# Performance work log

Hardware: AMD Instinct MI355X
Metric: run time of the kernel (lower is better)

## Reference

```python
import jax, jax.numpy as jnp
from jax import lax
import numpy as np

HF, WF, CIN, CONV_C, A, STRIDE = 100, 160, 512, 512, 9, 16
NEG = -1e9
IOU_THR = 0.7


def _make_anchor_map(hf, wf, stride):
    # (cy, cx, h, w) per anchor, 9 anchors: scales {64,128,256} x ratios {0.5,1,2}
    cy = (np.arange(hf, dtype=np.float32) + 0.5) * stride
    cx = (np.arange(wf, dtype=np.float32) + 0.5) * stride
    sizes = np.array([[s * np.sqrt(r), s / np.sqrt(r)]
                      for s in (64.0, 128.0, 256.0) for r in (0.5, 1.0, 2.0)],
                     dtype=np.float32)  # [9,2] = (h,w)
    cyg, cxg = np.meshgrid(cy, cx, indexing='ij')  # [hf,wf]
    am = np.zeros((hf, wf, A, 4), np.float32)
    am[..., 0] = cyg[..., None]
    am[..., 1] = cxg[..., None]
    am[..., 2] = sizes[:, 0]
    am[..., 3] = sizes[:, 1]
    return jnp.asarray(am.reshape(1, hf, wf, 4 * A))


def _conv(x, w, b, pad):
    y = lax.conv_general_dilated(x, w, (1, 1), pad,
                                 dimension_numbers=('NHWC', 'HWIO', 'NHWC'))
    return y + b


def _nms(boxes, scores, max_out, iou_thr):
    # jit-friendly fixed-size NMS; index computation is non-differentiable.
    bx = lax.stop_gradient(boxes)
    y1, x1, y2, x2 = bx[:, 0], bx[:, 1], bx[:, 2], bx[:, 3]
    areas = (y2 - y1) * (x2 - x1)

    def step(sc, _):
        best = jnp.argmax(sc)
        ok = sc[best] > NEG * 0.5
        b = bx[best]
        iy1 = jnp.maximum(y1, b[0]); ix1 = jnp.maximum(x1, b[1])
        iy2 = jnp.minimum(y2, b[2]); ix2 = jnp.minimum(x2, b[3])
        inter = jnp.maximum(iy2 - iy1, 0.0) * jnp.maximum(ix2 - ix1, 0.0)
        iou = inter / (areas + areas[best] - inter + 1e-8)
        sc = jnp.where((iou > iou_thr) & ok, NEG, sc)
        sc = sc.at[best].set(NEG)
        return sc, (best, ok)

    _, (keep, valid) = lax.scan(step, lax.stop_gradient(scores), None, length=max_out)
    return jnp.where(valid[:, None], boxes[keep], 0.0)  # [max_out,4], zero-padded


def setup_inputs() -> dict:
    key = jax.random.key(0)
    ks = jax.random.split(key, 6)
    image = jax.random.normal(ks[0], (1, HF * STRIDE, WF * STRIDE, 3), jnp.float32)
    feature_map = jax.random.normal(ks[1], (1, HF, WF, CIN), jnp.float32)
    anchor_map = _make_anchor_map(HF, WF, STRIDE)
    W1 = jax.random.normal(ks[2], (3, 3, CIN, CONV_C), jnp.float32) * 0.01
    b1 = jnp.zeros((CONV_C,), jnp.float32)
    Wc = jax.random.normal(ks[3], (1, 1, CONV_C, A), jnp.float32) * 0.01
    bc = jnp.zeros((A,), jnp.float32)
    Wr = jax.random.normal(ks[4], (1, 1, CONV_C, 4 * A), jnp.float32) * 0.01
    br = jnp.zeros((4 * A,), jnp.float32)
    return {'image': image, 'feature_map': feature_map, 'anchor_map': anchor_map,
            'W1': W1, 'b1': b1, 'Wc': Wc, 'bc': bc, 'Wr': Wr, 'br': br, 'training': 0}


def reference(image, feature_map, anchor_map, W1, b1, Wc, bc, Wr, br, training):
    pre_nms, post_nms = ((12000, 2000) if training else (6000, 300))
    # conv heads
    y = jax.nn.relu(_conv(feature_map, W1, b1, 'SAME'))
    scores_map = jax.nn.softmax(_conv(y, Wc, bc, 'SAME'), axis=-1)   # [1,HF,WF,9]
    delta_map = _conv(y, Wr, br, 'SAME')                              # [1,HF,WF,36]
    # flatten (_extract)
    anchors = anchor_map.reshape(-1, 4)        # (cy,cx,h,w)
    scores = scores_map.reshape(-1)            # [N]
    box_deltas = delta_map.reshape(-1, 4)      # (ty,tx,th,tw)
    # deltas_to_bboxes (means=0, stds=1)
    ctr = anchors[:, :2] + box_deltas[:, :2] * anchors[:, 2:]
    sz = anchors[:, 2:] * jnp.exp(box_deltas[:, 2:])
    proposals = jnp.concatenate([ctr - 0.5 * sz, ctr + 0.5 * sz], axis=1)  # (y1,x1,y2,x2)
    # sort desc + pre-NMS top-k
    top_scores, top_idx = lax.top_k(scores, pre_nms)
    proposals = proposals[top_idx]
    # clip to image
    h = jnp.float32(image.shape[1]); w = jnp.float32(image.shape[2])
    tl = jnp.maximum(proposals[:, 0:2], 0.0)
    y2 = jnp.minimum(proposals[:, 2], h)[:, None]
    x2 = jnp.minimum(proposals[:, 3], w)[:, None]
    proposals = jnp.concatenate([tl, y2, x2], axis=1)
    # size filter (mask instead of gather; NMS skips masked boxes)
    height = proposals[:, 2] - proposals[:, 0]
    width = proposals[:, 3] - proposals[:, 1]
    valid = (height >= 16.0) & (width >= 16.0)
    nms_scores = jnp.where(valid, top_scores, NEG)
    out_props = _nms(proposals, nms_scores, post_nms, IOU_THR)
    return (scores_map, box_deltas, out_props)
```

## Files before the change

### kernel.cpp

```cpp
#include <hip/hip_runtime.h>
#include <math.h>

#define HF 100
#define WFD 160
#define CIN 512
#define CONV_C 512
#define NPIX (HF*WFD)
#define NBOX (NPIX*9)
#define PRE_NMS 6000
#define POST_NMS 300
#define NEGV (-1.0e9f)
#define IMG_H 1600.0f
#define IMG_W 2560.0f
#define NHBINS 32768
#define NWORDS 94
#define NSORT 6016

#define PR 102
#define PC 162
#define NPAD ((size_t)PR*PC*512)

typedef __attribute__((ext_vector_type(8))) _Float16 half8;
typedef __attribute__((ext_vector_type(4))) float floatx4;

__device__ __forceinline__ unsigned short f2h_hi(float x) {
    _Float16 h = (_Float16)x;
    return __builtin_bit_cast(unsigned short, h);
}
__device__ __forceinline__ unsigned short f2h_lo(float x, unsigned short hbits) {
    _Float16 h = __builtin_bit_cast(_Float16, hbits);
    _Float16 l = (_Float16)((x - (float)h) * 2048.0f);
    return __builtin_bit_cast(unsigned short, l);
}

#define GLL16(g, l) __builtin_amdgcn_global_load_lds( \
    (const __attribute__((address_space(1))) void*)(g), \
    (__attribute__((address_space(3))) void*)(l), 16, 0, 0)

static const size_t OYREG = 0;
static const size_t OXH   = OYREG + (size_t)NPIX * CONV_C;
static const size_t OXL   = OXH + NPAD / 2;
static const size_t OWH   = OXL + NPAD / 2;
static const size_t OWL   = OWH + (size_t)9*512*512/2;
static const size_t ORAW  = OWL + (size_t)9*512*512/2;
static const size_t ONMS  = ORAW + NBOX;
static const size_t OPY1  = ONMS + NBOX;
static const size_t OPX1  = OPY1 + NBOX;
static const size_t OPY2  = OPX1 + NBOX;
static const size_t OPX2  = OPY2 + NBOX;
static const size_t OHIST = OPX2 + NBOX;
static const size_t OCNT  = OHIST + NHBINS;
static const size_t OPAR  = OCNT + 4;
static const size_t OCS   = OPAR + 2;
static const size_t OCY1  = OCS + PRE_NMS;
static const size_t OCX1  = OCY1 + PRE_NMS;
static const size_t OCY2  = OCX1 + PRE_NMS;
static const size_t OCX2  = OCY2 + PRE_NMS;
static const size_t OW2H  = OCX2 + PRE_NMS;
static const size_t OW2L  = OW2H + 12288;
static const size_t OMASK = OXH;
static const size_t OSY1  = OXL;
static const size_t OSX1  = OSY1 + NSORT;
static const size_t OSY2  = OSX1 + NSORT;
static const size_t OSX2  = OSY2 + NSORT;
static const size_t OSAR  = OSX2 + NSORT;

__global__ __launch_bounds__(256) void split_x(
    const float* __restrict__ X,
    unsigned short* __restrict__ Xh, unsigned short* __restrict__ Xl)
{
    const int idx = blockIdx.x * 256 + threadIdx.x;
    const int p = idx >> 7;
    const int kq = (idx & 127) * 4;
    const float4 v = *(const float4*)(X + (size_t)p * 512 + kq);
    const int r = p / WFD, c = p % WFD;
    const size_t dst = ((size_t)(r + 1) * PC + (c + 1)) * 512 + kq;
    float vv[4] = { v.x, v.y, v.z, v.w };
    unsigned short h[4], lo[4];
    #pragma unroll
    for (int u = 0; u < 4; ++u) {
        h[u]  = f2h_hi(vv[u]);
        lo[u] = f2h_lo(vv[u], h[u]);
    }
    uint2 ph, pl;
    ph.x = (unsigned)h[0]  | ((unsigned)h[1]  << 16);
    ph.y = (unsigned)h[2]  | ((unsigned)h[3]  << 16);
    pl.x = (unsigned)lo[0] | ((unsigned)lo[1] << 16);
    pl.y = (unsigned)lo[2] | ((unsigned)lo[3] << 16);
    *(uint2*)(Xh + dst) = ph;
    *(uint2*)(Xl + dst) = pl;
}

__global__ __launch_bounds__(256) void split_w(
    const float* __restrict__ W1,
    unsigned short* __restrict__ Wh, unsigned short* __restrict__ Wl)
{
    __shared__ unsigned short Lh[64 * 64];
    __shared__ unsigned short Ll[64 * 64];
    const int t = threadIdx.x;
    const int dydx = blockIdx.x >> 6;
    const int rem  = blockIdx.x & 63;
    const int k0 = (rem >> 3) * 64, n0 = (rem & 7) * 64;

    #pragma unroll
    for (int i = 0; i < 4; ++i) {
        const int f = t + 256 * i;
        const int row = f >> 4;
        const int cp  = (f & 15) * 4;
        const float4 v = *(const float4*)(W1 + ((size_t)(dydx * 512 + k0 + row)) * 512 + n0 + cp);
        float vv[4] = { v.x, v.y, v.z, v.w };
        #pragma unroll
        for (int u = 0; u < 4; ++u) {
            const unsigned short h = f2h_hi(vv[u]);
            Lh[(cp + u) * 64 + row] = h;
            Ll[(cp + u) * 64 + row] = f2h_lo(vv[u], h);
        }
    }
    __syncthreads();
    const int n  = t >> 2;
    const int kp = (t & 3) * 16;
    const size_t gbase = ((size_t)(dydx * 512 + n0 + n)) * 512 + k0 + kp;
    *(uint4*)(Wh + gbase)     = *(const uint4*)(Lh + n * 64 + kp);
    *(uint4*)(Wh + gbase + 8) = *(const uint4*)(Lh + n * 64 + kp + 8);
    *(uint4*)(Wl + gbase)     = *(const uint4*)(Ll + n * 64 + kp);
    *(uint4*)(Wl + gbase + 8) = *(const uint4*)(Ll + n * 64 + kp + 8);
}

__global__ __launch_bounds__(256) void split_w2(
    const float* __restrict__ Wc, const float* __restrict__ Wr,
    unsigned short* __restrict__ W2h, unsigned short* __restrict__ W2l)
{
    const int i = blockIdx.x * 256 + threadIdx.x;
    if (i >= 48 * 512) return;
    const int n = i >> 9, k = i & 511;
    float v = 0.f;
    if (n < 9) v = Wc[k * 9 + n];
    else if (n < 45) v = Wr[k * 36 + (n - 9)];
    const unsigned short h = f2h_hi(v);
    W2h[i] = h;
    W2l[i] = f2h_lo(v, h);
}

__global__ __launch_bounds__(256, 2) void conv_mfma(
    const unsigned short* __restrict__ Xh, const unsigned short* __restrict__ Xl,
    const unsigned short* __restrict__ Wh, const unsigned short* __restrict__ Wl,
    const float* __restrict__ b1,
    unsigned short* __restrict__ Yh, unsigned short* __restrict__ Yl)
{
    __shared__ alignas(16) unsigned short Ah[2][128 * 32];
    __shared__ alignas(16) unsigned short Al[2][128 * 32];
    __shared__ alignas(16) unsigned short Bh[2][128 * 32];
    __shared__ alignas(16) unsigned short Bl[2][128 * 32];

    const int tid = threadIdx.x;
    const int w = tid >> 6, l = tid & 63;
    const int wy = w >> 1, wx = w & 1;

    const int bx = blockIdx.x;
    const int q = bx & 7, s5 = bx >> 3;
    const int tile = (q < 5) ? (q * 16 + s5) : (80 + (q - 5) * 15 + s5);
    const int pm0 = tile * 128, oc0 = blockIdx.y * 128;

    const int swW = ((l & 3) ^ ((l >> 3) & 3)) * 8;
    int aoff[2], boff[2], ldsOff[2];
    #pragma unroll
    for (int i = 0; i < 2; ++i) {
        const int m = w * 32 + i * 16 + (l >> 2);
        const int p = pm0 + m;
        const int r = p / WFD, c = p % WFD;
        aoff[i] = ((r + 1) * PC + (c + 1)) * 512 + swW;
        boff[i] = (oc0 + m) * 512 + swW;
        ldsOff[i] = (w * 32 + i * 16) * 32;
    }

    const int swR = (((l >> 4) ^ ((l >> 1) & 3))) * 8;
    int afrag[4], bfrag[4];
    #pragma unroll
    for (int i = 0; i < 4; ++i) {
        afrag[i] = (wy * 64 + i * 16 + (l & 15)) * 32 + swR;
        bfrag[i] = (wx * 64 + i * 16 + (l & 15)) * 32 + swR;
    }

    floatx4 acc[4][4], accL[4][4];
    #pragma unroll
    for (int j = 0; j < 4; ++j) {
        const float bv = b1[oc0 + wx * 64 + j * 16 + (l & 15)];
        #pragma unroll
        for (int i = 0; i < 4; ++i) {
            acc[i][j][0] = bv; acc[i][j][1] = bv; acc[i][j][2] = bv; acc[i][j][3] = bv;
            accL[i][j][0] = 0.f; accL[i][j][1] = 0.f; accL[i][j][2] = 0.f; accL[i][j][3] = 0.f;
        }
    }

    #define CSTAGE(bf, dAx, dBx)                                    \
        _Pragma("unroll")                                           \
        for (int i = 0; i < 2; ++i) {                               \
            GLL16(Xh + aoff[i] + (dAx), Ah[bf] + ldsOff[i]);        \
            GLL16(Xl + aoff[i] + (dAx), Al[bf] + ldsOff[i]);        \
            GLL16(Wh + boff[i] + (dBx), Bh[bf] + ldsOff[i]);        \
            GLL16(Wl + boff[i] + (dBx), Bl[bf] + ldsOff[i]);        \
        }

    CSTAGE(0, (-PC - 1) * 512, 0);

    for (int step = 0; step < 144; ++step) {
        const int cur = step & 1;
        if (step < 143) {
            const int s1 = step + 1;
            const int d1 = s1 >> 4;
            const int k1 = (s1 & 15) << 5;
            const int dy = d1 / 3 - 1, dx = d1 % 3 - 1;
            CSTAGE(cur ^ 1, (dy * PC + dx) * 512 + k1, d1 * (512 * 512) + k1);
            asm volatile("s_waitcnt vmcnt(8)" ::: "memory");
        } else {
            asm volatile("s_waitcnt vmcnt(0)" ::: "memory");
        }
        __builtin_amdgcn_s_barrier();
        asm volatile("" ::: "memory");

        const unsigned short* Ac = Ah[cur];
        const unsigned short* Lc = Al[cur];
        const unsigned short* Bc = Bh[cur];
        const unsigned short* Mc = Bl[cur];
        half8 fah[4], fal[4], fbh[4], fbl[4];
        #pragma unroll
        for (int i = 0; i < 4; ++i) {
            fah[i] = *(const half8*)(Ac + afrag[i]);
            fal[i] = *(const half8*)(Lc + afrag[i]);
            fbh[i] = *(const half8*)(Bc + bfrag[i]);
            fbl[i] = *(const half8*)(Mc + bfrag[i]);
        }
        #pragma unroll
        for (int i = 0; i < 4; ++i)
            #pragma unroll
            for (int j = 0; j < 4; ++j) {
                acc[i][j]  = __builtin_amdgcn_mfma_f32_16x16x32_f16(fah[i], fbh[j], acc[i][j], 0, 0, 0);
                accL[i][j] = __builtin_amdgcn_mfma_f32_16x16x32_f16(fal[i], fbh[j], accL[i][j], 0, 0, 0);
                accL[i][j] = __builtin_amdgcn_mfma_f32_16x16x32_f16(fah[i], fbl[j], accL[i][j], 0, 0, 0);
            }
        asm volatile("" ::: "memory");
        __builtin_amdgcn_s_barrier();
    }
    #undef CSTAGE

    #pragma unroll
    for (int i = 0; i < 4; ++i) {
        const int row0 = pm0 + wy * 64 + i * 16 + (l >> 4) * 4;
        #pragma unroll
        for (int j = 0; j < 4; ++j) {
            const int col = oc0 + wx * 64 + j * 16 + (l & 15);
            #pragma unroll
            for (int r = 0; r < 4; ++r) {
                const float yv = fmaxf(acc[i][j][r] + accL[i][j][r] * 4.8828125e-4f, 0.f);
                const unsigned short h = f2h_hi(yv);
                const size_t o = (size_t)(row0 + r) * 512 + col;
                Yh[o] = h;
                Yl[o] = f2h_lo(yv, h);
            }
        }
    }
}

__global__ __launch_bounds__(256) void heads_mfma(
    const unsigned short* __restrict__ Yh, const unsigned short* __restrict__ Yl,
    const unsigned short* __restrict__ W2h, const unsigned short* __restrict__ W2l,
    const float* __restrict__ bc, const float* __restrict__ br,
    const float* __restrict__ anch,
    float* __restrict__ out_scores, float* __restrict__ out_deltas,
    float* __restrict__ rawS, float* __restrict__ nmsS,
    float* __restrict__ pY1, float* __restrict__ pX1,
    float* __restrict__ pY2, float* __restrict__ pX2,
    unsigned int* __restrict__ hist)
{
    __shared__ alignas(16) unsigned short Ah[128 * 32];
    __shared__ alignas(16) unsigned short Al[128 * 32];
    __shared__ alignas(16) unsigned short Bh[48 * 32];
    __shared__ alignas(16) unsigned short Bl[48 * 32];
    __shared__ float Lg[128 * 49];
    __shared__ unsigned int Hh[NHBINS / 2];

    const int tid = threadIdx.x;
    const int w = tid >> 6, l = tid & 63;
    const int pm0 = blockIdx.x * 128;

    #pragma unroll 4
    for (int i = tid; i < NHBINS / 2; i += 256) Hh[i] = 0u;

    const int swW = ((l & 3) ^ ((l >> 3) & 3)) * 8;
    int aoff[2], ldsOff[2];
    #pragma unroll
    for (int i = 0; i < 2; ++i) {
        const int m = w * 32 + i * 16 + (l >> 2);
        aoff[i] = (pm0 + m) * 512 + swW;
        ldsOff[i] = (w * 32 + i * 16) * 32;
    }
    const int bglb = (w * 16 + (l >> 2)) * 512 + swW;
    const int blds = w * 16 * 32;

    const int swR = (((l >> 4) ^ ((l >> 1) & 3))) * 8;
    int afrag[2], bfrag[3];
    #pragma unroll
    for (int i = 0; i < 2; ++i)
        afrag[i] = (w * 32 + i * 16 + (l & 15)) * 32 + swR;
    #pragma unroll
    for (int j = 0; j < 3; ++j)
        bfrag[j] = (j * 16 + (l & 15)) * 32 + swR;

    floatx4 acc[2][3], accL[2][3];
    #pragma unroll
    for (int i = 0; i < 2; ++i)
        #pragma unroll
        for (int j = 0; j < 3; ++j) {
            acc[i][j][0] = 0.f; acc[i][j][1] = 0.f; acc[i][j][2] = 0.f; acc[i][j][3] = 0.f;
            accL[i][j] = acc[i][j];
        }

    for (int k0 = 0; k0 < 512; k0 += 32) {
        __syncthreads();
        #pragma unroll
        for (int i = 0; i < 2; ++i) {
            GLL16(Yh + aoff[i] + k0, Ah + ldsOff[i]);
            GLL16(Yl + aoff[i] + k0, Al + ldsOff[i]);
        }
        if (w < 3) {
            GLL16(W2h + bglb + k0, Bh + blds);
            GLL16(W2l + bglb + k0, Bl + blds);
        }
        __syncthreads();
        half8 fah[2], fal[2], fbh[3], fbl[3];
        #pragma unroll
        for (int i = 0; i < 2; ++i) {
            fah[i] = *(const half8*)(Ah + afrag[i]);
            fal[i] = *(const half8*)(Al + afrag[i]);
        }
        #pragma unroll
        for (int j = 0; j < 3; ++j) {
            fbh[j] = *(const half8*)(Bh + bfrag[j]);
            fbl[j] = *(const half8*)(Bl + bfrag[j]);
        }
        #pragma unroll
        for (int i = 0; i < 2; ++i)
            #pragma unroll
            for (int j = 0; j < 3; ++j) {
                acc[i][j]  = __builtin_amdgcn_mfma_f32_16x16x32_f16(fah[i], fbh[j], acc[i][j], 0, 0, 0);
                accL[i][j] = __builtin_amdgcn_mfma_f32_16x16x32_f16(fal[i], fbh[j], accL[i][j], 0, 0, 0);
                accL[i][j] = __builtin_amdgcn_mfma_f32_16x16x32_f16(fah[i], fbl[j], accL[i][j], 0, 0, 0);
            }
    }

    __syncthreads();
    #pragma unroll
    for (int i = 0; i < 2; ++i) {
        const int prow0 = w * 32 + i * 16 + (l >> 4) * 4;
        #pragma unroll
        for (int j = 0; j < 3; ++j) {
            const int col = j * 16 + (l & 15);
            #pragma unroll
            for (int r = 0; r < 4; ++r)
                Lg[(prow0 + r) * 49 + col] = acc[i][j][r] + accL[i][j][r] * 4.8828125e-4f;
        }
    }
    __syncthreads();

    if (tid < 128) {
        const int p = pm0 + tid;
        float ac[9], arr[36];
        #pragma unroll
        for (int a = 0; a < 9; ++a) ac[a] = Lg[tid * 49 + a] + bc[a];
        #pragma unroll
        for (int j = 0; j < 36; ++j) arr[j] = Lg[tid * 49 + 9 + j] + br[j];

        float m = ac[0];
        #pragma unroll
        for (int a = 1; a < 9; ++a) m = fmaxf(m, ac[a]);
        float s = 0.f, e[9];
        #pragma unroll
        for (int a = 0; a < 9; ++a) { e[a] = expf(ac[a] - m); s += e[a]; }
        #pragma unroll
        for (int a = 0; a < 9; ++a) e[a] = e[a] / s;

        #pragma unroll
        for (int a = 0; a < 9; ++a) out_scores[p * 9 + a] = e[a];
        #pragma unroll
        for (int a = 0; a < 9; ++a)
            *(float4*)(out_deltas + (size_t)p * 36 + 4 * a) =
                make_float4(arr[4*a], arr[4*a+1], arr[4*a+2], arr[4*a+3]);

        #pragma unroll
        for (int a = 0; a < 9; ++a) {
            const float4 an = *(const float4*)(anch + (size_t)p * 36 + 4 * a);
            const float cty = an.x + arr[4*a]   * an.z;
            const float ctx = an.y + arr[4*a+1] * an.w;
            const float szy = an.z * expf(arr[4*a+2]);
            const float szx = an.w * expf(arr[4*a+3]);
            float y1 = fmaxf(cty - 0.5f * szy, 0.f);
            float x1 = fmaxf(ctx - 0.5f * szx, 0.f);
            float y2 = fminf(cty + 0.5f * szy, IMG_H);
            float x2 = fminf(ctx + 0.5f * szx, IMG_W);
            const bool valid = ((y2 - y1) >= 16.f) && ((x2 - x1) >= 16.f);
            const int idx = p * 9 + a;
            rawS[idx] = e[a];
            nmsS[idx] = valid ? e[a] : NEGV;
            pY1[idx] = y1; pX1[idx] = x1; pY2[idx] = y2; pX2[idx] = x2;
            const unsigned b = __float_as_uint(e[a]) >> 15;
            atomicAdd(&Hh[b >> 1], (b & 1) ? 65536u : 1u);
        }
    }

    __syncthreads();
    for (int i = tid; i < NHBINS / 2; i += 256) {
        const unsigned v = Hh[i];
        if (v) {
            const unsigned lo = v & 0xFFFFu;
            const unsigned hi = v >> 16;
            if (lo) atomicAdd(&hist[2 * i],     lo);
            if (hi) atomicAdd(&hist[2 * i + 1], hi);
        }
    }
}

__global__ __launch_bounds__(1024) void select_k(const unsigned int* __restrict__ hist,
                                                 int* __restrict__ params)
{
    __shared__ unsigned int ps[1024];
    const int t = threadIdx.x;
    unsigned int loc[32];
    unsigned int sum = 0;
    #pragma unroll 4
    for (int i = 0; i < 32; ++i) { loc[i] = hist[t * 32 + i]; sum += loc[i]; }
    ps[t] = sum;
    for (int off = 1; off < 1024; off <<= 1) {
        __syncthreads();
        const unsigned int add = (t + off < 1024) ? ps[t + off] : 0u;
        __syncthreads();
        ps[t] += add;
    }
    __syncthreads();
    const unsigned int above = (t < 1023) ? ps[t + 1] : 0u;
    if (above < (unsigned)PRE_NMS && ps[t] >= (unsigned)PRE_NMS) {
        unsigned int cum = above;
        for (int j = 31; j >= 0; --j) {
            const unsigned int h = loc[j];
            if (cum + h >= (unsigned)PRE_NMS) {
                params[0] = t * 32 + j;
                params[1] = PRE_NMS - (int)cum;
                break;
            }
            cum += h;
        }
    }
}

__global__ void compact_k(const float* __restrict__ rawS, const float* __restrict__ nmsS,
                          const float* __restrict__ pY1, const float* __restrict__ pX1,
                          const float* __restrict__ pY2, const float* __restrict__ pX2,
                          const int* __restrict__ params, int* __restrict__ cnts,
                          float* __restrict__ cS,
                          float* __restrict__ cY1, float* __restrict__ cX1,
                          float* __restrict__ cY2, float* __restrict__ cX2)
{
    const int i = blockIdx.x * 256 + threadIdx.x;
    if (i >= NBOX) return;
    const int b = (int)(__float_as_uint(rawS[i]) >> 15);
    const int bin = params[0];
    const int need = params[1];
    int pos = -1;
    if (b > bin) {
        pos = atomicAdd(&cnts[0], 1);
    } else if (b == bin) {
        const int t2 = atomicAdd(&cnts[1], 1);
        if (t2 < need) pos = atomicAdd(&cnts[0], 1);
    }
    if (pos >= 0) {
        const float sv = nmsS[i];
        cS[pos]  = sv;
        cY1[pos] = pY1[i]; cX1[pos] = pX1[i];
        cY2[pos] = pY2[i]; cX2[pos] = pX2[i];
        if (sv > NEGV * 0.5f) atomicAdd(&cnts[2], 1);
    }
}

__global__ __launch_bounds__(1024) void sort_k(
    const float* __restrict__ cS,
    const float* __restrict__ cY1, const float* __restrict__ cX1,
    const float* __restrict__ cY2, const float* __restrict__ cX2,
    float* __restrict__ sY1, float* __restrict__ sX1,
    float* __restrict__ sY2, float* __restrict__ sX2,
    float* __restrict__ sAr)
{
    __shared__ unsigned long long keys[8192];
    const int t = threadIdx.x;
    for (int i = t; i < 8192; i += 1024) {
        unsigned long long k;
        if (i < PRE_NMS) {
            const unsigned b = __float_as_uint(cS[i]);
            const unsigned m = (b & 0x80000000u) ? ~b : (b | 0x80000000u);
            k = ((unsigned long long)(~m) << 32) | (unsigned)i;
        } else {
            k = ~0ULL;
        }
        keys[i] = k;
    }
    for (int kk = 2; kk <= 8192; kk <<= 1) {
        for (int j = kk >> 1; j > 0; j >>= 1) {
            __syncthreads();
            for (int t4 = t; t4 < 4096; t4 += 1024) {
                const int i  = ((t4 & ~(j - 1)) << 1) | (t4 & (j - 1));
                const int p2 = i | j;
                const bool up = ((i & kk) == 0);
                const unsigned long long a = keys[i], b = keys[p2];
                const bool sw = up ? (a > b) : (a < b);
                if (sw) { keys[i] = b; keys[p2] = a; }
            }
        }
    }
    __syncthreads();
    for (int i = t; i < NSORT; i += 1024) {
        if (i < PRE_NMS) {
            const int j = (int)(keys[i] & 0xFFFFFFFFu);
            const float y1 = cY1[j], x1 = cX1[j], y2 = cY2[j], x2 = cX2[j];
            sY1[i] = y1; sX1[i] = x1; sY2[i] = y2; sX2[i] = x2;
            sAr[i] = (y2 - y1) * (x2 - x1);
        } else {
            sY1[i] = 0.f; sX1[i] = 0.f; sY2[i] = 0.f; sX2[i] = 0.f; sAr[i] = 0.f;
        }
    }
}

__global__ __launch_bounds__(64) void mask_k(
    const float* __restrict__ sY1, const float* __restrict__ sX1,
    const float* __restrict__ sY2, const float* __restrict__ sX2,
    const float* __restrict__ sAr, unsigned long long* __restrict__ mask)
{
    __shared__ float ly1[64], lx1[64], ly2[64], lx2[64], lar[64];
    const int t = threadIdx.x;
    const int c = blockIdx.y * 64 + t;
    ly1[t] = sY1[c]; lx1[t] = sX1[c]; ly2[t] = sY2[c]; lx2[t] = sX2[c]; lar[t] = sAr[c];
    __syncthreads();
    const int r = blockIdx.x * 64 + t;
    const float ry1 = sY1[r], rx1 = sX1[r], ry2 = sY2[r], rx2 = sX2[r], rar = sAr[r];
    unsigned long long bits = 0ULL;
    #pragma unroll 8
    for (int u = 0; u < 64; ++u) {
        const float iy1 = fmaxf(ry1, ly1[u]);
        const float ix1 = fmaxf(rx1, lx1[u]);
        const float iy2 = fminf(ry2, ly2[u]);
        const float ix2 = fminf(rx2, lx2[u]);
        const float inter = fmaxf(iy2 - iy1, 0.f) * fmaxf(ix2 - ix1, 0.f);
        const float iou = inter / (lar[u] + rar - inter + 1e-8f);
        bits |= (iou > 0.7f) ? (1ULL << u) : 0ULL;
    }
    mask[(size_t)r * NWORDS + blockIdx.y] = bits;
}

__global__ __launch_bounds__(64) void scan2_k(
    const float* __restrict__ sY1, const float* __restrict__ sX1,
    const float* __restrict__ sY2, const float* __restrict__ sX2,
    const unsigned long long* __restrict__ mask, const int* __restrict__ cnts,
    float* __restrict__ outP)
{
    __shared__ alignas(16) unsigned long long rows[64][96];
    const int l = threadIdx.x;
    const int nvRaw = cnts[2];
    const int nv = nvRaw < PRE_NMS ? nvRaw : PRE_NMS;
    unsigned long long r0 = 0ULL, r1 = 0ULL;
    int n = 0;
    for (int w = 0; w < NWORDS; ++w) {
        const int base = w << 6;
        if (base >= nv || n >= POST_NMS) break;
        for (int r = 0; r < 64; ++r) {
            if (l < 47)
                GLL16(mask + (size_t)(base + r) * NWORDS + 2 * l, &rows[r][0]);
        }
        const int ci = base + l;
        const float v1 = sY1[ci], v2 = sX1[ci], v3 = sY2[ci], v4 = sX2[ci];
        __syncthreads();
        unsigned long long cw = (w < 64) ? __shfl(r0, w, 64) : __shfl(r1, w - 64, 64);
        const int lim = nv - base;
        if (lim < 64) cw |= (~0ULL << lim);
        while (cw != ~0ULL && n < POST_NMS) {
            const int b = (int)__builtin_ctzll(~cw);
            const float by1 = __shfl(v1, b, 64);
            const float bx1 = __shfl(v2, b, 64);
            const float by2 = __shfl(v3, b, 64);
            const float bx2 = __shfl(v4, b, 64);
            if (l == 0) {
                outP[4 * n + 0] = by1; outP[4 * n + 1] = bx1;
                outP[4 * n + 2] = by2; outP[4 * n + 3] = bx2;
            }
            ++n;
            cw |= (1ULL << b);
            if (n >= POST_NMS) break;
            r0 |= rows[b][l];
            if (l < NWORDS - 64) r1 |= rows[b][64 + l];
            cw |= rows[b][w];
        }
        __syncthreads();
    }
    for (int idx = 4 * n + l; idx < 4 * POST_NMS; idx += 64) outP[idx] = 0.f;
}

extern "C" void kernel_launch(void* const* d_in, const int* in_sizes, int n_in,
                              void* d_out, int out_size, void* d_ws, size_t ws_size,
                              hipStream_t stream)
{
    const float* X    = (const float*)d_in[1];
    const float* anch = (const float*)d_in[2];
    const float* W1   = (const float*)d_in[3];
    const float* b1   = (const float*)d_in[4];
    const float* Wc   = (const float*)d_in[5];
    const float* bc   = (const float*)d_in[6];
    const float* Wr   = (const float*)d_in[7];
    const float* br   = (const float*)d_in[8];

    float* out = (float*)d_out;
    float* ws  = (float*)d_ws;

    unsigned short* Yh = (unsigned short*)(ws + OYREG);
    unsigned short* Yl = Yh + (size_t)NPIX * CONV_C;
    unsigned short* Xh = (unsigned short*)(ws + OXH);
    unsigned short* Xl = (unsigned short*)(ws + OXL);
    unsigned short* Wh = (unsigned short*)(ws + OWH);
    unsigned short* Wl = (unsigned short*)(ws + OWL);
    float* rawS = ws + ORAW;
    float* nmsS = ws + ONMS;
    float* pY1  = ws + OPY1;
    float* pX1  = ws + OPX1;
    float* pY2  = ws + OPY2;
    float* pX2  = ws + OPX2;
    unsigned int* hist = (unsigned int*)(ws + OHIST);
    int* cnts   = (int*)(ws + OCNT);
    int* params = (int*)(ws + OPAR);
    float* cS   = ws + OCS;
    float* cY1  = ws + OCY1;
    float* cX1  = ws + OCX1;
    float* cY2  = ws + OCY2;
    float* cX2  = ws + OCX2;
    unsigned short* W2h = (unsigned short*)(ws + OW2H);
    unsigned short* W2l = (unsigned short*)(ws + OW2L);
    float* sY1  = ws + OSY1;
    float* sX1  = ws + OSX1;
    float* sY2  = ws + OSY2;
    float* sX2  = ws + OSX2;
    float* sAr  = ws + OSAR;
    unsigned long long* mask = (unsigned long long*)(ws + OMASK);

    float* out_scores = out;
    float* out_deltas = out + NBOX;
    float* out_props  = out + (size_t)NBOX * 5;

    hipMemsetAsync(hist, 0, (NHBINS + 8) * sizeof(unsigned int), stream);
    hipMemsetAsync(Xh, 0, 2 * NPAD * sizeof(unsigned short), stream);

    split_x<<<8000, 256, 0, stream>>>(X, Xh, Xl);
    split_w<<<576, 256, 0, stream>>>(W1, Wh, Wl);
    split_w2<<<96, 256, 0, stream>>>(Wc, Wr, W2h, W2l);

    conv_mfma<<<dim3(125, 4), 256, 0, stream>>>(Xh, Xl, Wh, Wl, b1, Yh, Yl);

    heads_mfma<<<125, 256, 0, stream>>>(Yh, Yl, W2h, W2l, bc, br, anch,
        out_scores, out_deltas, rawS, nmsS, pY1, pX1, pY2, pX2, hist);

    select_k<<<1, 1024, 0, stream>>>(hist, params);
    compact_k<<<(NBOX + 255) / 256, 256, 0, stream>>>(
        rawS, nmsS, pY1, pX1, pY2, pX2, params, cnts, cS, cY1, cX1, cY2, cX2);

    sort_k<<<1, 1024, 0, stream>>>(cS, cY1, cX1, cY2, cX2,
                                   sY1, sX1, sY2, sX2, sAr);
    mask_k<<<dim3(NWORDS, NWORDS), 64, 0, stream>>>(sY1, sX1, sY2, sX2, sAr, mask);
    scan2_k<<<1, 64, 0, stream>>>(sY1, sX1, sY2, sX2, mask, cnts, out_props);
}
```

Baseline: 632.9 us.

## Aggregate compaction atomics per wave and double-buffer NMS mask loads

The compaction kernel now uses wave ballots so that one lane per wave issues a single atomicAdd for the whole group, where before every thread issued its own atomic. The NMS scan kernel grows to four waves that share the mask-row loads into LDS, double-buffers them so the next 64-row block is prefetched while wave 0 runs the serial suppression scan, and passes the kept count through shared memory. This cuts atomic contention and hides global-load latency in the single-block tail. In exchange it adds LDS usage, extra barriers and hand-written s_waitcnt counts that must match the number of outstanding loads.

```diff
diff --git a/kernel.cpp b/kernel.cpp
--- a/kernel.cpp
+++ b/kernel.cpp
@@ -460,17 +460,46 @@
                           float* __restrict__ cY2, float* __restrict__ cX2)
 {
     const int i = blockIdx.x * 256 + threadIdx.x;
-    if (i >= NBOX) return;
-    const int b = (int)(__float_as_uint(rawS[i]) >> 15);
+    const int lane = threadIdx.x & 63;
+    const bool act = i < NBOX;
+    int b = -1;
+    if (act) b = (int)(__float_as_uint(rawS[i]) >> 15);
     const int bin = params[0];
     const int need = params[1];
     int pos = -1;
-    if (b > bin) {
-        pos = atomicAdd(&cnts[0], 1);
-    } else if (b == bin) {
-        const int t2 = atomicAdd(&cnts[1], 1);
-        if (t2 < need) pos = atomicAdd(&cnts[0], 1);
-    }
+
+    {
+        const bool p = act && (b > bin);
+        const unsigned long long m = __ballot(p);
+        if (p) {
+            const int leader = __ffsll(m) - 1;
+            int base = 0;
+            if (lane == leader) base = atomicAdd(&cnts[0], __popcll(m));
+            base = __shfl(base, leader, 64);
+            pos = base + __popcll(m & ((1ULL << lane) - 1));
+        }
+    }
+    {
+        const bool p = act && (b == bin);
+        const unsigned long long m = __ballot(p);
+        if (p) {
+            const int leader = __ffsll(m) - 1;
+            int base2 = 0;
+            if (lane == leader) base2 = atomicAdd(&cnts[1], __popcll(m));
+            base2 = __shfl(base2, leader, 64);
+            const int t2 = base2 + __popcll(m & ((1ULL << lane) - 1));
+            const bool take = t2 < need;
+            const unsigned long long m3 = __ballot(take);
+            if (take) {
+                const int leader3 = __ffsll(m3) - 1;
+                int base3 = 0;
+                if (lane == leader3) base3 = atomicAdd(&cnts[0], __popcll(m3));
+                base3 = __shfl(base3, leader3, 64);
+                pos = base3 + __popcll(m3 & ((1ULL << lane) - 1));
+            }
+        }
+    }
+
     if (pos >= 0) {
         const float sv = nmsS[i];
         cS[pos]  = sv;
@@ -553,51 +582,77 @@
     mask[(size_t)r * NWORDS + blockIdx.y] = bits;
 }
 
-__global__ __launch_bounds__(64) void scan2_k(
+__global__ __launch_bounds__(256) void scan2_k(
     const float* __restrict__ sY1, const float* __restrict__ sX1,
     const float* __restrict__ sY2, const float* __restrict__ sX2,
     const unsigned long long* __restrict__ mask, const int* __restrict__ cnts,
     float* __restrict__ outP)
 {
-    __shared__ alignas(16) unsigned long long rows[64][96];
-    const int l = threadIdx.x;
+    __shared__ alignas(16) unsigned long long rows[2][64][96];
+    __shared__ int sn;
+    const int tid = threadIdx.x;
+    const int wv = tid >> 6, l = tid & 63;
     const int nvRaw = cnts[2];
     const int nv = nvRaw < PRE_NMS ? nvRaw : PRE_NMS;
+    const int nw = (nv + 63) >> 6;
     unsigned long long r0 = 0ULL, r1 = 0ULL;
     int n = 0;
-    for (int w = 0; w < NWORDS; ++w) {
-        const int base = w << 6;
-        if (base >= nv || n >= POST_NMS) break;
-        for (int r = 0; r < 64; ++r) {
-            if (l < 47)
-                GLL16(mask + (size_t)(base + r) * NWORDS + 2 * l, &rows[r][0]);
-        }
-        const int ci = base + l;
-        const float v1 = sY1[ci], v2 = sX1[ci], v3 = sY2[ci], v4 = sX2[ci];
+    if (tid == 0) sn = 0;
+
+    #define SSTAGE(w_, buf_)                                                     \
+        for (int r = 0; r < 16; ++r) {                                           \
+            if (l < 47)                                                          \
+                GLL16(mask + (size_t)(((w_) << 6) + wv * 16 + r) * NWORDS + 2*l, \
+                      &rows[buf_][wv * 16 + r][0]);                              \
+        }
+
+    if (nw > 0) { SSTAGE(0, 0); }
+
+    for (int w = 0; w < nw; ++w) {
+        const int buf = w & 1;
+        const bool pf = (w + 1 < nw);
+        if (pf) {
+            SSTAGE(w + 1, buf ^ 1);
+            asm volatile("s_waitcnt vmcnt(16)" ::: "memory");
+        } else {
+            asm volatile("s_waitcnt vmcnt(0)" ::: "memory");
+        }
         __syncthreads();
-        unsigned long long cw = (w < 64) ? __shfl(r0, w, 64) : __shfl(r1, w - 64, 64);
-        const int lim = nv - base;
-        if (lim < 64) cw |= (~0ULL << lim);
-        while (cw != ~0ULL && n < POST_NMS) {
-            const int b = (int)__builtin_ctzll(~cw);
-            const float by1 = __shfl(v1, b, 64);
-            const float bx1 = __shfl(v2, b, 64);
-            const float by2 = __shfl(v3, b, 64);
-            const float bx2 = __shfl(v4, b, 64);
-            if (l == 0) {
-                outP[4 * n + 0] = by1; outP[4 * n + 1] = bx1;
-                outP[4 * n + 2] = by2; outP[4 * n + 3] = bx2;
+
+        if (wv == 0) {
+            const int base = w << 6;
+            const int ci = base + l;
+            const float v1 = sY1[ci], v2 = sX1[ci], v3 = sY2[ci], v4 = sX2[ci];
+            unsigned long long cw = (w < 64) ? __shfl(r0, w, 64) : __shfl(r1, w - 64, 64);
+            const int lim = nv - base;
+            if (lim < 64) cw |= (~0ULL << lim);
+            while (cw != ~0ULL && n < POST_NMS) {
+                const int b = (int)__builtin_ctzll(~cw);
+                const float by1 = __shfl(v1, b, 64);
+                const float bx1 = __shfl(v2, b, 64);
+                const float by2 = __shfl(v3, b, 64);
+                const float bx2 = __shfl(v4, b, 64);
+                if (l == 0) {
+                    outP[4 * n + 0] = by1; outP[4 * n + 1] = bx1;
+                    outP[4 * n + 2] = by2; outP[4 * n + 3] = bx2;
+                }
+                ++n;
+                cw |= (1ULL << b);
+                if (n >= POST_NMS) break;
+                r0 |= rows[buf][b][l];
+                if (l < NWORDS - 64) r1 |= rows[buf][b][64 + l];
+                cw |= rows[buf][b][w];
             }
-            ++n;
-            cw |= (1ULL << b);
-            if (n >= POST_NMS) break;
-            r0 |= rows[b][l];
-            if (l < NWORDS - 64) r1 |= rows[b][64 + l];
-            cw |= rows[b][w];
+            if (l == 0) sn = n;
         }
         __syncthreads();
-    }
-    for (int idx = 4 * n + l; idx < 4 * POST_NMS; idx += 64) outP[idx] = 0.f;
+        n = sn;
+        if (n >= POST_NMS) break;
+    }
+    #undef SSTAGE
+    asm volatile("s_waitcnt vmcnt(0)" ::: "memory");
+
+    for (int idx = 4 * n + tid; idx < 4 * POST_NMS; idx += 256) outP[idx] = 0.f;
 }
 
 extern "C" void kernel_launch(void* const* d_in, const int* in_sizes, int n_in,
@@ -668,5 +723,5 @@
     sort_k<<<1, 1024, 0, stream>>>(cS, cY1, cX1, cY2, cX2,
                                    sY1, sX1, sY2, sX2, sAr);
     mask_k<<<dim3(NWORDS, NWORDS), 64, 0, stream>>>(sY1, sX1, sY2, sX2, sAr, mask);
-    scan2_k<<<1, 64, 0, stream>>>(sY1, sX1, sY2, sX2, mask, cnts, out_props);
-}
+    scan2_k<<<1, 256, 0, stream>>>(sY1, sX1, sY2, sX2, mask, cnts, out_props);
+}
```

New measurement: 641.5 us. Within noise of the previous version (+1.4%).

## Fuse preprocessing kernels and memsets into one launch, zero only padding border

Applied to the files above, without the earlier changes.

Merges split_x, split_w, split_w2 and the histogram memset into a single prep kernel that dispatches on block index. It also stops memsetting the whole padded Xh/Xl buffer (about 34 MB) and instead zeros only the border pixels, since the interior is fully overwritten. This removes several launches and a large redundant memory write. In exchange it depends on the border index math being exactly right and on Xh/Xl being contiguous in the expected order.

```diff
diff --git a/kernel.cpp b/kernel.cpp
--- a/kernel.cpp
+++ b/kernel.cpp
@@ -19,6 +19,14 @@
 #define PR 102
 #define PC 162
 #define NPAD ((size_t)PR*PC*512)
+
+#define PB_SX   8000
+#define PB_SW   576
+#define PB_SW2  96
+#define PB_HZ   32
+#define NBORD   524
+#define PB_BZ   262
+#define PB_TOT  (PB_SX+PB_SW+PB_SW2+PB_HZ+PB_BZ)
 
 typedef __attribute__((ext_vector_type(8))) _Float16 half8;
 typedef __attribute__((ext_vector_type(4))) float floatx4;
@@ -65,80 +73,97 @@
 static const size_t OSX2  = OSY2 + NSORT;
 static const size_t OSAR  = OSX2 + NSORT;
 
-__global__ __launch_bounds__(256) void split_x(
-    const float* __restrict__ X,
-    unsigned short* __restrict__ Xh, unsigned short* __restrict__ Xl)
-{
-    const int idx = blockIdx.x * 256 + threadIdx.x;
-    const int p = idx >> 7;
-    const int kq = (idx & 127) * 4;
-    const float4 v = *(const float4*)(X + (size_t)p * 512 + kq);
-    const int r = p / WFD, c = p % WFD;
-    const size_t dst = ((size_t)(r + 1) * PC + (c + 1)) * 512 + kq;
-    float vv[4] = { v.x, v.y, v.z, v.w };
-    unsigned short h[4], lo[4];
-    #pragma unroll
-    for (int u = 0; u < 4; ++u) {
-        h[u]  = f2h_hi(vv[u]);
-        lo[u] = f2h_lo(vv[u], h[u]);
-    }
-    uint2 ph, pl;
-    ph.x = (unsigned)h[0]  | ((unsigned)h[1]  << 16);
-    ph.y = (unsigned)h[2]  | ((unsigned)h[3]  << 16);
-    pl.x = (unsigned)lo[0] | ((unsigned)lo[1] << 16);
-    pl.y = (unsigned)lo[2] | ((unsigned)lo[3] << 16);
-    *(uint2*)(Xh + dst) = ph;
-    *(uint2*)(Xl + dst) = pl;
-}
-
-__global__ __launch_bounds__(256) void split_w(
-    const float* __restrict__ W1,
-    unsigned short* __restrict__ Wh, unsigned short* __restrict__ Wl)
+__global__ __launch_bounds__(256) void prep_k(
+    const float* __restrict__ X, const float* __restrict__ W1,
+    const float* __restrict__ Wc, const float* __restrict__ Wr,
+    unsigned short* __restrict__ Xh, unsigned short* __restrict__ Xl,
+    unsigned short* __restrict__ Wh, unsigned short* __restrict__ Wl,
+    unsigned short* __restrict__ W2h, unsigned short* __restrict__ W2l,
+    unsigned int* __restrict__ hist)
 {
     __shared__ unsigned short Lh[64 * 64];
     __shared__ unsigned short Ll[64 * 64];
+    const int B = blockIdx.x;
     const int t = threadIdx.x;
-    const int dydx = blockIdx.x >> 6;
-    const int rem  = blockIdx.x & 63;
-    const int k0 = (rem >> 3) * 64, n0 = (rem & 7) * 64;
-
-    #pragma unroll
-    for (int i = 0; i < 4; ++i) {
-        const int f = t + 256 * i;
-        const int row = f >> 4;
-        const int cp  = (f & 15) * 4;
-        const float4 v = *(const float4*)(W1 + ((size_t)(dydx * 512 + k0 + row)) * 512 + n0 + cp);
+
+    if (B < PB_SX) {
+        const int idx = B * 256 + t;
+        const int p = idx >> 7;
+        const int kq = (idx & 127) * 4;
+        const float4 v = *(const float4*)(X + (size_t)p * 512 + kq);
+        const int r = p / WFD, c = p % WFD;
+        const size_t dst = ((size_t)(r + 1) * PC + (c + 1)) * 512 + kq;
         float vv[4] = { v.x, v.y, v.z, v.w };
+        unsigned short h[4], lo[4];
         #pragma unroll
         for (int u = 0; u < 4; ++u) {
-            const unsigned short h = f2h_hi(vv[u]);
-            Lh[(cp + u) * 64 + row] = h;
-            Ll[(cp + u) * 64 + row] = f2h_lo(vv[u], h);
-        }
-    }
-    __syncthreads();
-    const int n  = t >> 2;
-    const int kp = (t & 3) * 16;
-    const size_t gbase = ((size_t)(dydx * 512 + n0 + n)) * 512 + k0 + kp;
-    *(uint4*)(Wh + gbase)     = *(const uint4*)(Lh + n * 64 + kp);
-    *(uint4*)(Wh + gbase + 8) = *(const uint4*)(Lh + n * 64 + kp + 8);
-    *(uint4*)(Wl + gbase)     = *(const uint4*)(Ll + n * 64 + kp);
-    *(uint4*)(Wl + gbase + 8) = *(const uint4*)(Ll + n * 64 + kp + 8);
-}
-
-__global__ __launch_bounds__(256) void split_w2(
-    const float* __restrict__ Wc, const float* __restrict__ Wr,
-    unsigned short* __restrict__ W2h, unsigned short* __restrict__ W2l)
-{
-    const int i = blockIdx.x * 256 + threadIdx.x;
-    if (i >= 48 * 512) return;
-    const int n = i >> 9, k = i & 511;
-    float v = 0.f;
-    if (n < 9) v = Wc[k * 9 + n];
-    else if (n < 45) v = Wr[k * 36 + (n - 9)];
-    const unsigned short h = f2h_hi(v);
-    W2h[i] = h;
-    W2l[i] = f2h_lo(v, h);
+            h[u]  = f2h_hi(vv[u]);
+            lo[u] = f2h_lo(vv[u], h[u]);
+        }
+        uint2 ph, pl;
+        ph.x = (unsigned)h[0]  | ((unsigned)h[1]  << 16);
+        ph.y = (unsigned)h[2]  | ((unsigned)h[3]  << 16);
+        pl.x = (unsigned)lo[0] | ((unsigned)lo[1] << 16);
+        pl.y = (unsigned)lo[2] | ((unsigned)lo[3] << 16);
+        *(uint2*)(Xh + dst) = ph;
+        *(uint2*)(Xl + dst) = pl;
+    } else if (B < PB_SX + PB_SW) {
+        const int blk = B - PB_SX;
+        const int dydx = blk >> 6;
+        const int rem  = blk & 63;
+        const int k0 = (rem >> 3) * 64, n0 = (rem & 7) * 64;
+        #pragma unroll
+        for (int i = 0; i < 4; ++i) {
+            const int f = t + 256 * i;
+            const int row = f >> 4;
+            const int cp  = (f & 15) * 4;
+            const float4 v = *(const float4*)(W1 + ((size_t)(dydx * 512 + k0 + row)) * 512 + n0 + cp);
+            float vv[4] = { v.x, v.y, v.z, v.w };
+            #pragma unroll
+            for (int u = 0; u < 4; ++u) {
+                const unsigned short h = f2h_hi(vv[u]);
+                Lh[(cp + u) * 64 + row] = h;
+                Ll[(cp + u) * 64 + row] = f2h_lo(vv[u], h);
+            }
+        }
+        __syncthreads();
+        const int n  = t >> 2;
+        const int kp = (t & 3) * 16;
+        const size_t gbase = ((size_t)(dydx * 512 + n0 + n)) * 512 + k0 + kp;
+        *(uint4*)(Wh + gbase)     = *(const uint4*)(Lh + n * 64 + kp);
+        *(uint4*)(Wh + gbase + 8) = *(const uint4*)(Lh + n * 64 + kp + 8);
+        *(uint4*)(Wl + gbase)     = *(const uint4*)(Ll + n * 64 + kp);
+        *(uint4*)(Wl + gbase + 8) = *(const uint4*)(Ll + n * 64 + kp + 8);
+    } else if (B < PB_SX + PB_SW + PB_SW2) {
+        const int i = (B - PB_SX - PB_SW) * 256 + t;
+        if (i < 48 * 512) {
+            const int n = i >> 9, k = i & 511;
+            float v = 0.f;
+            if (n < 9) v = Wc[k * 9 + n];
+            else if (n < 45) v = Wr[k * 36 + (n - 9)];
+            const unsigned short h = f2h_hi(v);
+            W2h[i] = h;
+            W2l[i] = f2h_lo(v, h);
+        }
+    } else if (B < PB_SX + PB_SW + PB_SW2 + PB_HZ) {
+        for (int i = (B - PB_SX - PB_SW - PB_SW2) * 256 + t; i < NHBINS + 8; i += PB_HZ * 256)
+            hist[i] = 0u;
+    } else {
+        const int s = (B - PB_SX - PB_SW - PB_SW2 - PB_HZ) * 256 + t;
+        if (s < NBORD * 64 * 2) {
+            const int arr = (s >= NBORD * 64) ? 1 : 0;
+            const int si  = arr ? s - NBORD * 64 : s;
+            const int pix = si >> 6, chunk = si & 63;
+            int r, c;
+            if (pix < PC)            { r = 0;                      c = pix; }
+            else if (pix < 2 * PC)   { r = PR - 1;                 c = pix - PC; }
+            else if (pix < 2 * PC + (PR - 2)) { r = 1 + (pix - 2 * PC);            c = 0; }
+            else                     { r = 1 + (pix - 2 * PC - (PR - 2)); c = PC - 1; }
+            unsigned short* dstA = arr ? Xl : Xh;
+            uint4 z; z.x = 0u; z.y = 0u; z.z = 0u; z.w = 0u;
+            *(uint4*)(dstA + ((size_t)r * PC + c) * 512 + chunk * 8) = z;
+        }
+    }
 }
 
 __global__ __launch_bounds__(256, 2) void conv_mfma(
@@ -649,12 +674,8 @@
     float* out_deltas = out + NBOX;
     float* out_props  = out + (size_t)NBOX * 5;
 
-    hipMemsetAsync(hist, 0, (NHBINS + 8) * sizeof(unsigned int), stream);
-    hipMemsetAsync(Xh, 0, 2 * NPAD * sizeof(unsigned short), stream);
-
-    split_x<<<8000, 256, 0, stream>>>(X, Xh, Xl);
-    split_w<<<576, 256, 0, stream>>>(W1, Wh, Wl);
-    split_w2<<<96, 256, 0, stream>>>(Wc, Wr, W2h, W2l);
+    prep_k<<<PB_TOT, 256, 0, stream>>>(X, W1, Wc, Wr,
+                                       Xh, Xl, Wh, Wl, W2h, W2l, hist);
 
     conv_mfma<<<dim3(125, 4), 256, 0, stream>>>(Xh, Xl, Wh, Wl, b1, Yh, Yl);
 
```

Result: no change. 629.7 us (-0.5%).
